# Kernel optimization log

Hardware: AMD Instinct MI355X
Metric: run time of the kernel (lower is better)

## Reference

```python
import jax, jax.numpy as jnp
import numpy as np

B, L, D, H = 2, 4096, 1024, 4
DK = D // H
DV = D // H
CHUNK, FIRS, FIRL, CONV, GROUP = 32, 3, 31, 4, 2
EPS_ID, R_EPS = 0.06, 0.025   # step==0 -> router epsilon at its start value
R_HID = 2 * D
R_IN = D + H * 6


def _l2norm(x, eps=1e-6):
    return x * jax.lax.rsqrt(jnp.sum(x * x, -1, keepdims=True) + eps)


def _causal_dwconv(x, w):
    # x: (b, l, c), w: (c, k); depthwise causal conv1d
    c = x.shape[-1]
    k = w.shape[-1]
    lhs = jnp.swapaxes(x, 1, 2)              # (b, c, l)
    rhs = w[:, None, :]                      # (c, 1, k)
    y = jax.lax.conv_general_dilated(lhs, rhs, window_strides=(1,), padding=[(k - 1, 0)],
                                     dimension_numbers=('NCH', 'OIH', 'NCH'), feature_group_count=c)
    return jnp.swapaxes(y, 1, 2)


def _fir(x, filt):
    # x: (b, l, h, d), filt: (h, d, k) depthwise causal FIR per head-channel
    b, l, h, d = x.shape
    y = _causal_dwconv(x.reshape(b, l, h * d), filt.reshape(h * d, -1))
    return y.reshape(b, l, h, d)


def _delta_rule_chunkwise(q, k, v, beta, chunk=CHUNK):
    # q,k: (b,h,L,dk)  v: (b,h,L,dv)  beta: (b,h,L); L % chunk == 0
    b, h, Ls, dk = q.shape
    dv = v.shape[-1]
    n = Ls // chunk
    q = _l2norm(q)
    k = _l2norm(k)
    v = v * beta[..., None]
    kb = k * beta[..., None]
    rs = lambda t: t.reshape(b, h, n, chunk, -1)
    q, k, v, kb = map(rs, (q, k, v, kb))
    tri = jnp.triu(jnp.ones((chunk, chunk), bool), 0)
    # UT transform: forward substitution to invert (I + strictly-lower(K_beta K^T))
    T = jnp.where(tri, 0.0, -(kb @ jnp.swapaxes(k, -1, -2)))
    for i in range(1, chunk):
        T = T.at[..., i, :].add(jnp.einsum('...j,...jl->...l', T[..., i, :], T))
    T = T + jnp.eye(chunk, dtype=T.dtype)
    u = T @ v          # (b,h,n,c,dv)
    w = T @ kb         # (b,h,n,c,dk)
    fmask = jnp.triu(jnp.ones((chunk, chunk), bool), 1)
    mv = lambda t: jnp.moveaxis(t, 2, 0)

    def step(S, xs):
        qi, ki, ui, wi = xs
        attn = jnp.where(fmask, 0.0, qi @ jnp.swapaxes(ki, -1, -2))
        u2 = ui - wi @ S
        oi = qi @ S + attn @ u2
        return S + jnp.swapaxes(ki, -1, -2) @ u2, oi

    S0 = jnp.zeros((b, h, dk, dv), q.dtype)
    S, o = jax.lax.scan(step, S0, (mv(q), mv(k), mv(u), mv(w)))
    return jnp.moveaxis(o, 0, 2).reshape(b, h, Ls, dv), S


def setup_inputs():
    key = jax.random.key(0)
    ks = jax.random.split(key, 20)
    lin = lambda kk, i, o: 0.02 * jax.random.normal(kk, (i, o), jnp.float32)

    def fir(kk, kern):
        base = jnp.zeros((H, DV, kern), jnp.float32).at[:, :, -1].set(1.0)
        return base + 0.01 * jax.random.normal(kk, (H, DV, kern), jnp.float32)

    return {
        'hidden_states': jax.random.normal(ks[0], (B, L, D), jnp.float32),
        'Wq': lin(ks[1], D, H * DK), 'Wk': lin(ks[2], D, H * DK), 'Wv': lin(ks[3], D, H * DV),
        'Wb': lin(ks[4], D, H),
        'conv_q': 0.3 * jax.random.normal(ks[5], (H * DK, CONV), jnp.float32),
        'conv_k': 0.3 * jax.random.normal(ks[6], (H * DK, CONV), jnp.float32),
        'conv_v': 0.3 * jax.random.normal(ks[7], (H * DV, CONV), jnp.float32),
        'fir_short': fir(ks[8], FIRS), 'fir_long': fir(ks[9], FIRL),
        'alpha_id': jnp.zeros((H,), jnp.float32),
        'Wid': lin(ks[10], D, H), 'bid': jnp.zeros((H,), jnp.float32),
        'Wr1': lin(ks[11], R_IN, R_HID), 'br1': jnp.zeros((R_HID,), jnp.float32),
        'Wr2': lin(ks[12], R_HID, H * 3), 'br2': jnp.zeros((H * 3,), jnp.float32),
        'log_tau_group': jnp.zeros(((H + GROUP - 1) // GROUP,), jnp.float32),
        'log_tau_head': jnp.zeros((H,), jnp.float32),
        'o_norm_w': jnp.ones((DV,), jnp.float32),
        'Wo': lin(ks[13], H * DV, D),
    }


def reference(hidden_states, Wq, Wk, Wv, Wb, conv_q, conv_k, conv_v, fir_short, fir_long,
              alpha_id, Wid, bid, Wr1, br1, Wr2, br2, log_tau_group, log_tau_head, o_norm_w, Wo):
    x = hidden_states
    b, l = x.shape[:2]
    # projections + causal short conv + silu (qk_activation='silu')
    q = jax.nn.silu(_causal_dwconv(x @ Wq, conv_q))
    k = jax.nn.silu(_causal_dwconv(x @ Wk, conv_k))
    v = jax.nn.silu(_causal_dwconv(x @ Wv, conv_v))
    qh = q.reshape(b, l, H, DK)
    kh = k.reshape(b, l, H, DK)
    vh = v.reshape(b, l, H, DV)
    beta = jax.nn.sigmoid(x @ Wb)                      # (b,l,h)
    bhld = lambda t: jnp.transpose(t, (0, 2, 1, 3))
    delta, _S = _delta_rule_chunkwise(bhld(qh), bhld(kh), bhld(vh), jnp.transpose(beta, (0, 2, 1)))
    delta = jnp.transpose(delta, (0, 2, 1, 3))         # (b,l,h,dv)
    fs = _fir(vh, fir_short)
    fl = _fir(vh, fir_long)
    # per-head mean/std stats of the three branch outputs
    stats = jnp.concatenate([fs.mean(-1), fs.std(-1), fl.mean(-1), fl.std(-1),
                             delta.mean(-1), delta.std(-1)], -1)   # (b,l,6h)
    router_in = jnp.concatenate([x, stats], -1)
    hmid = jax.nn.gelu(router_in @ Wr1 + br1, approximate=False)
    logits = (hmid @ Wr2 + br2).reshape(b, l, H, 3)
    group_idx = jnp.arange(H) // GROUP
    # step==0 -> mix=1.0: tau is the per-group temperature
    tau = jnp.exp(log_tau_group)[group_idx] + 0.0 * jnp.exp(log_tau_head)
    p = jax.nn.softmax(logits / tau[None, None, :, None], -1)
    p = p * (1.0 - 3.0 * R_EPS) + R_EPS                # epsilon-floor
    o = p[..., 0:1] * fs + p[..., 1:2] * fl + p[..., 2:3] * delta
    # gated identity (value) path
    id_scale = EPS_ID + jax.nn.sigmoid(alpha_id)[None, None, :] * jax.nn.sigmoid(x @ Wid + bid)
    o = o + id_scale[..., None] * vh
    # per-head RMSNorm then output projection
    o = o * jax.lax.rsqrt(jnp.mean(o * o, -1, keepdims=True) + 1e-5) * o_norm_w
    return o.reshape(b, l, H * DV) @ Wo
```

## Files before the change

kernel.cpp:

```cpp
#include <hip/hip_runtime.h>
#include <hip/hip_bf16.h>
#include <math.h>

#define BATCH 2
#define SEQ 4096
#define DMODEL 1024
#define NH 4
#define DHEAD 256
#define NCHUNK 128
#define ROWS (BATCH * SEQ)

typedef short s8v __attribute__((ext_vector_type(8)));
typedef float f4v __attribute__((ext_vector_type(4)));

__device__ __forceinline__ float sigm(float x) { return 1.0f / (1.0f + expf(-x)); }
__device__ __forceinline__ float siluf(float x) { return x / (1.0f + expf(-x)); }
__device__ __forceinline__ unsigned short f2b(float f) {
  __hip_bfloat16 h = __float2bfloat16(f);
  return *(unsigned short*)&h;
}

__global__ __launch_bounds__(256) void cast_bf16(
    const float* __restrict__ in, __hip_bfloat16* __restrict__ out) {
  long i = ((long)blockIdx.x * 256 + threadIdx.x) * 4;
  float4 v = *(const float4*)(in + i);
  __hip_bfloat16 tmp[4] = {__float2bfloat16(v.x), __float2bfloat16(v.y),
                           __float2bfloat16(v.z), __float2bfloat16(v.w)};
  *(ushort4*)(out + i) = *(ushort4*)tmp;
}

__global__ __launch_bounds__(256) void transpose_cast(
    const float* __restrict__ W, __hip_bfloat16* __restrict__ Wt,
    int K, int N, int Ks) {
  __shared__ float tile[32][33];
  const int t = threadIdx.x;
  const int tx = t & 31, ty = t >> 5;
  const int kb = blockIdx.y * 32, nb = blockIdx.x * 32;
#pragma unroll
  for (int r = 0; r < 4; ++r) {
    int kk = kb + ty + 8 * r;
    tile[ty + 8 * r][tx] = (kk < K) ? W[(long)kk * N + nb + tx] : 0.f;
  }
  __syncthreads();
#pragma unroll
  for (int r = 0; r < 4; ++r) {
    Wt[(long)(nb + ty + 8 * r) * Ks + kb + tx] = __float2bfloat16(tile[tx][ty + 8 * r]);
  }
}

__global__ __launch_bounds__(256) void fir_transpose(
    const float* __restrict__ fshort, const float* __restrict__ flong,
    float* __restrict__ fsT, float* __restrict__ flT) {
  const int j = blockIdx.x;
  const int t = threadIdx.x;
  if (j < 31) {
#pragma unroll
    for (int i = 0; i < 4; ++i) {
      int c = t * 4 + i;
      flT[j * 1024 + c] = flong[c * 31 + j];
    }
  } else {
    int tp = j - 31;
#pragma unroll
    for (int i = 0; i < 4; ++i) {
      int c = t * 4 + i;
      fsT[tp * 1024 + c] = fshort[c * 3 + tp];
    }
  }
}

template <int ACT, bool BF16OUT>
__global__ __launch_bounds__(256) void gemm_bf16(
    const __hip_bfloat16* __restrict__ A, const __hip_bfloat16* __restrict__ Bt,
    const float* __restrict__ bias, void* __restrict__ Cv,
    int M, int N, int Ks) {
  __shared__ short As[128 * 32];
  __shared__ short Bs[128 * 32];
  const int t = threadIdx.x;
  const int wv = t >> 6;
  const int lane = t & 63;
  const int row0 = blockIdx.y * 128, col0 = blockIdx.x * 128;
  const int mq = (wv >> 1) * 64, nq = (wv & 1) * 64;
  const int ln15 = lane & 15;
  const int kq = (lane >> 4) * 8;
  const int sr = t >> 2;
  const int sc = (t & 3) * 8;
  const short* Ag = (const short*)A + (long)(row0 + sr) * Ks + sc;
  const short* Bg = (const short*)Bt + (long)(col0 + sr) * Ks + sc;
  const long rstep = (long)64 * Ks;

  f4v acc[4][4];
#pragma unroll
  for (int i = 0; i < 4; ++i)
#pragma unroll
    for (int j = 0; j < 4; ++j) acc[i][j] = (f4v){0.f, 0.f, 0.f, 0.f};

  uint4 a0 = *(const uint4*)(Ag);
  uint4 a1 = *(const uint4*)(Ag + rstep);
  uint4 b0 = *(const uint4*)(Bg);
  uint4 b1 = *(const uint4*)(Bg + rstep);
  for (int k0 = 0; k0 < Ks; k0 += 32) {
    __syncthreads();
    *(uint4*)&As[sr * 32 + sc] = a0;
    *(uint4*)&As[(sr + 64) * 32 + sc] = a1;
    *(uint4*)&Bs[sr * 32 + sc] = b0;
    *(uint4*)&Bs[(sr + 64) * 32 + sc] = b1;
    __syncthreads();
    if (k0 + 32 < Ks) {
      a0 = *(const uint4*)(Ag + k0 + 32);
      a1 = *(const uint4*)(Ag + rstep + k0 + 32);
      b0 = *(const uint4*)(Bg + k0 + 32);
      b1 = *(const uint4*)(Bg + rstep + k0 + 32);
    }
    s8v af[4], bf[4];
#pragma unroll
    for (int mt = 0; mt < 4; ++mt)
      af[mt] = *(const s8v*)&As[(mq + mt * 16 + ln15) * 32 + kq];
#pragma unroll
    for (int nt = 0; nt < 4; ++nt)
      bf[nt] = *(const s8v*)&Bs[(nq + nt * 16 + ln15) * 32 + kq];
#pragma unroll
    for (int mt = 0; mt < 4; ++mt)
#pragma unroll
      for (int nt = 0; nt < 4; ++nt)
        acc[mt][nt] = __builtin_amdgcn_mfma_f32_16x16x32_bf16(af[mt], bf[nt], acc[mt][nt], 0, 0, 0);
  }
  const int rbase = (lane >> 4) * 4;
#pragma unroll
  for (int mt = 0; mt < 4; ++mt) {
#pragma unroll
    for (int nt = 0; nt < 4; ++nt) {
      int gcol = col0 + nq + nt * 16 + ln15;
#pragma unroll
      for (int r = 0; r < 4; ++r) {
        int grow = row0 + mq + mt * 16 + rbase + r;
        float v = acc[mt][nt][r];
        if (ACT == 1) {
          v += bias[gcol];
          v = 0.5f * v * (1.0f + erff(v * 0.70710678118654752f));
        }
        if (BF16OUT) {
          ((__hip_bfloat16*)Cv)[(long)grow * N + gcol] = __float2bfloat16(v);
        } else {
          ((float*)Cv)[(long)grow * N + gcol] = v;
        }
      }
    }
  }
}

__global__ __launch_bounds__(256) void rowdot8(
    const float* __restrict__ x, const float* __restrict__ Wb,
    const float* __restrict__ Wid, const float* __restrict__ alpha_id,
    const float* __restrict__ bidp, float* __restrict__ beta, float* __restrict__ idsc) {
  const int row = blockIdx.x;
  const int t = threadIdx.x;
  const float* xr = x + (long)row * DMODEL;
  float ab[4] = {0, 0, 0, 0}, ai[4] = {0, 0, 0, 0};
  for (int k = t; k < DMODEL; k += 256) {
    float xv = xr[k];
    float4 wb = *(const float4*)(Wb + k * 4);
    float4 wi = *(const float4*)(Wid + k * 4);
    ab[0] = fmaf(xv, wb.x, ab[0]); ab[1] = fmaf(xv, wb.y, ab[1]);
    ab[2] = fmaf(xv, wb.z, ab[2]); ab[3] = fmaf(xv, wb.w, ab[3]);
    ai[0] = fmaf(xv, wi.x, ai[0]); ai[1] = fmaf(xv, wi.y, ai[1]);
    ai[2] = fmaf(xv, wi.z, ai[2]); ai[3] = fmaf(xv, wi.w, ai[3]);
  }
#pragma unroll
  for (int m = 1; m < 64; m <<= 1) {
#pragma unroll
    for (int hh = 0; hh < 4; ++hh) {
      ab[hh] += __shfl_xor(ab[hh], m);
      ai[hh] += __shfl_xor(ai[hh], m);
    }
  }
  __shared__ float red[4][8];
  if ((t & 63) == 0) {
    int wv = t >> 6;
#pragma unroll
    for (int hh = 0; hh < 4; ++hh) {
      red[wv][hh] = ab[hh];
      red[wv][4 + hh] = ai[hh];
    }
  }
  __syncthreads();
  if (t < 8) {
    float s = red[0][t] + red[1][t] + red[2][t] + red[3][t];
    if (t < 4) {
      beta[(long)row * NH + t] = sigm(s);
    } else {
      int hh = t - 4;
      idsc[(long)row * NH + hh] = 0.06f + sigm(alpha_id[hh]) * sigm(s + bidp[hh]);
    }
  }
}

__global__ __launch_bounds__(256) void conv_silu(
    const float* __restrict__ pre, const float* __restrict__ cw, float* __restrict__ out) {
  const int row = blockIdx.x;
  const int l = row & (SEQ - 1);
  const int t = threadIdx.x;
  const int cb = t * 4;
  float wts[4][4];
#pragma unroll
  for (int cc = 0; cc < 4; ++cc) {
    float4 w4 = *(const float4*)(cw + (cb + cc) * 4);
    wts[cc][0] = w4.x; wts[cc][1] = w4.y; wts[cc][2] = w4.z; wts[cc][3] = w4.w;
  }
  float acc[4] = {0, 0, 0, 0};
#pragma unroll
  for (int tap = 0; tap < 4; ++tap) {
    int lr = l - 3 + tap;
    if (lr >= 0) {
      float4 xv = *(const float4*)(pre + (long)(row - 3 + tap) * DMODEL + cb);
      acc[0] = fmaf(wts[0][tap], xv.x, acc[0]);
      acc[1] = fmaf(wts[1][tap], xv.y, acc[1]);
      acc[2] = fmaf(wts[2][tap], xv.z, acc[2]);
      acc[3] = fmaf(wts[3][tap], xv.w, acc[3]);
    }
  }
  float4 ov = make_float4(siluf(acc[0]), siluf(acc[1]), siluf(acc[2]), siluf(acc[3]));
  *(float4*)(out + (long)row * DMODEL + cb) = ov;
}

__global__ __launch_bounds__(256) void l2norm_qk(
    float* __restrict__ q, float* __restrict__ k, __hip_bfloat16* __restrict__ qpk) {
  const int t = threadIdx.x;
  const int unit = blockIdx.x * 4 + (t >> 6);
  const int lane = t & 63;
  const int row = unit >> 2;
  const int h = unit & 3;
  const int b = row >> 12;
  const int l = row & (SEQ - 1);
  const long base = (long)row * DMODEL + h * DHEAD + lane * 4;
  float4 q4 = *(const float4*)(q + base);
  float4 k4 = *(const float4*)(k + base);
  float sq = q4.x * q4.x + q4.y * q4.y + q4.z * q4.z + q4.w * q4.w;
  float sk = k4.x * k4.x + k4.y * k4.y + k4.z * k4.z + k4.w * k4.w;
#pragma unroll
  for (int m = 1; m < 64; m <<= 1) {
    sq += __shfl_xor(sq, m);
    sk += __shfl_xor(sk, m);
  }
  float rq = rsqrtf(sq + 1e-6f);
  float rk = rsqrtf(sk + 1e-6f);
  q4.x *= rq; q4.y *= rq; q4.z *= rq; q4.w *= rq;
  k4.x *= rk; k4.y *= rk; k4.z *= rk; k4.w *= rk;
  *(float4*)(q + base) = q4;
  *(float4*)(k + base) = k4;
  ushort4 qb;
  qb.x = f2b(q4.x); qb.y = f2b(q4.y); qb.z = f2b(q4.z); qb.w = f2b(q4.w);
  *(ushort4*)(qpk + ((long)(b * NH + h) * SEQ + l) * DHEAD + lane * 4) = qb;
}

__global__ __launch_bounds__(256) void phaseA(
    const float* __restrict__ qn, const float* __restrict__ kn, const float* __restrict__ v,
    const float* __restrict__ beta, float* __restrict__ u,
    __hip_bfloat16* __restrict__ wb16, __hip_bfloat16* __restrict__ kTb16,
    __hip_bfloat16* __restrict__ attnb16) {
  __shared__ float Ks[32][256];
  __shared__ float T[32][33];
  __shared__ float bet[32];
  const int bid = blockIdx.x;
  const int c = bid & (NCHUNK - 1);
  const int h = (bid >> 7) & 3;
  const int b = bid >> 9;
  const int bh = b * NH + h;
  const int l0 = c * 32;
  const int t = threadIdx.x;
  const int wv = t >> 6;
  const int lane = t & 63;

#pragma unroll
  for (int r = 0; r < 8; ++r) {
    int idx = t + 256 * r;
    int i = idx >> 6;
    int f = (idx & 63) * 4;
    long gq = ((long)(b * SEQ + l0 + i)) * DMODEL + h * DHEAD + f;
    *(float4*)&Ks[i][f] = *(const float4*)(kn + gq);
  }
  if (t < 32) bet[t] = beta[(long)(b * SEQ + l0 + t) * NH + h];
  __syncthreads();

  {
#pragma unroll
    for (int ii = 0; ii < 8; ++ii) {
      const int i = wv * 8 + ii;
      float4 a = *(const float4*)&Ks[i][lane * 4];
      float nbi = -bet[i];
      for (int j = 0; j < 32; ++j) {
        float val = 0.f;
        if (j < i) {
          float4 bb = *(const float4*)&Ks[j][lane * 4];
          float pd = a.x * bb.x + a.y * bb.y + a.z * bb.z + a.w * bb.w;
#pragma unroll
          for (int m = 1; m < 64; m <<= 1) pd += __shfl_xor(pd, m);
          val = nbi * pd;
        }
        if (lane == 0) T[i][j] = val;
      }
    }
  }
  __syncthreads();

  if (t < 32) {
    const int l = t;
    for (int i = 1; i < 32; ++i) {
      float s = 0.f;
      for (int j = 0; j < i; ++j) s = fmaf(T[i][j], T[j][l], s);
      T[i][l] += s;
    }
    for (int i = 0; i < 32; ++i) {
      float val = T[i][l] + (i == l ? 1.f : 0.f);
      T[i][l] = val * bet[l];
    }
  }
  __syncthreads();

  {
    const int d = t;
    float acc[32];
#pragma unroll
    for (int i = 0; i < 32; ++i) acc[i] = 0.f;
    for (int j = 0; j < 32; ++j) {
      float vv = v[((long)(b * SEQ + l0 + j)) * DMODEL + h * DHEAD + d];
#pragma unroll
      for (int i = 0; i < 32; ++i) acc[i] = fmaf(T[i][j], vv, acc[i]);
    }
    long ubase = ((long)bh * SEQ + l0) * DHEAD + d;
#pragma unroll
    for (int i = 0; i < 32; ++i) u[ubase + (long)i * DHEAD] = acc[i];
#pragma unroll
    for (int i = 0; i < 32; ++i) acc[i] = 0.f;
    for (int j = 0; j < 32; ++j) {
      float kv = Ks[j][d];
#pragma unroll
      for (int i = 0; i < 32; ++i) acc[i] = fmaf(T[i][j], kv, acc[i]);
    }
#pragma unroll
    for (int i = 0; i < 32; ++i) wb16[ubase + (long)i * DHEAD] = __float2bfloat16(acc[i]);
  }

  {
    const int s = t;
    unsigned short* kb = (unsigned short*)kTb16 + ((long)bh * NCHUNK + c) * 8192 + (long)s * 32;
#pragma unroll
    for (int i4 = 0; i4 < 8; ++i4) {
      ushort4 pk;
      pk.x = f2b(Ks[i4 * 4 + 0][s]);
      pk.y = f2b(Ks[i4 * 4 + 1][s]);
      pk.z = f2b(Ks[i4 * 4 + 2][s]);
      pk.w = f2b(Ks[i4 * 4 + 3][s]);
      *(ushort4*)(kb + i4 * 4) = pk;
    }
  }

  {
    long abase = ((long)bh * NCHUNK + c) * 1024;
#pragma unroll
    for (int ii = 0; ii < 8; ++ii) {
      const int i = wv * 8 + ii;
      const float* qrow = qn + ((long)(b * SEQ + l0 + i)) * DMODEL + h * DHEAD;
      float4 a = *(const float4*)(qrow + lane * 4);
      for (int j = 0; j < 32; ++j) {
        float val = 0.f;
        if (j <= i) {
          float4 bb = *(const float4*)&Ks[j][lane * 4];
          float pd = a.x * bb.x + a.y * bb.y + a.z * bb.z + a.w * bb.w;
#pragma unroll
          for (int m = 1; m < 64; m <<= 1) pd += __shfl_xor(pd, m);
          val = pd;
        }
        if (lane == 0) attnb16[abase + i * 32 + j] = __float2bfloat16(val);
      }
    }
  }
}

__global__ __launch_bounds__(64, 1) void phaseB(
    const __hip_bfloat16* __restrict__ qpk,
    const __hip_bfloat16* __restrict__ wb,
    const __hip_bfloat16* __restrict__ kTb,
    const __hip_bfloat16* __restrict__ attnb,
    const float* __restrict__ u, float* __restrict__ delta ) {
  __shared__ __align__(16) short St[16 * 264];
  __shared__ __align__(16) short Ut[16 * 40];
  const int bid = blockIdx.x;
  const int slice = bid & 15;
  const int bh = bid >> 4;
  const int d0 = slice * 16;
  const int t = threadIdx.x;
  const int ln15 = t & 15;
  const int qw = t >> 4;

  const short* wbase = (const short*)wb + (long)bh * SEQ * 256;
  const short* qbase = (const short*)qpk + (long)bh * SEQ * 256;
  const short* kTbase = (const short*)kTb + (long)bh * NCHUNK * 8192;
  const short* atbase = (const short*)attnb + (long)bh * NCHUNK * 1024;
  const float* ubase = u + (long)bh * SEQ * 256;
  float* dbase = delta + (long)bh * SEQ * 256;

  f4v Sacc[16];
#pragma unroll
  for (int kt = 0; kt < 16; ++kt) Sacc[kt] = (f4v){0.f, 0.f, 0.f, 0.f};

  s8v wA[2][8], kA[16], atv[2];
  float uf[2][4];
  {
#pragma unroll
    for (int mt = 0; mt < 2; ++mt)
#pragma unroll
      for (int ks = 0; ks < 8; ++ks)
        wA[mt][ks] = *(const s8v*)(wbase + (long)(mt * 16 + ln15) * 256 + ks * 32 + qw * 8);
#pragma unroll
    for (int kt = 0; kt < 16; ++kt)
      kA[kt] = *(const s8v*)(kTbase + (kt * 16 + ln15) * 32 + qw * 8);
#pragma unroll
    for (int mt = 0; mt < 2; ++mt) {
      atv[mt] = *(const s8v*)(atbase + (mt * 16 + ln15) * 32 + qw * 8);
#pragma unroll
      for (int r = 0; r < 4; ++r)
        uf[mt][r] = ubase[(long)(mt * 16 + qw * 4 + r) * 256 + d0 + ln15];
    }
  }

  for (int c = 0; c < NCHUNK; ++c) {
    const int l0 = c * 32;

    s8v qA[2][8];
#pragma unroll
    for (int mt = 0; mt < 2; ++mt)
#pragma unroll
      for (int ks = 0; ks < 8; ++ks)
        qA[mt][ks] = *(const s8v*)(qbase + (long)(l0 + mt * 16 + ln15) * 256 + ks * 32 + qw * 8);

#pragma unroll
    for (int kt = 0; kt < 16; ++kt) {
      ushort4 pk;
      pk.x = f2b(Sacc[kt][0]); pk.y = f2b(Sacc[kt][1]);
      pk.z = f2b(Sacc[kt][2]); pk.w = f2b(Sacc[kt][3]);
      *(ushort4*)&St[ln15 * 264 + kt * 16 + qw * 4] = pk;
    }
    asm volatile("s_waitcnt lgkmcnt(0)" ::: "memory");
    s8v bS[8];
#pragma unroll
    for (int ks = 0; ks < 8; ++ks)
      bS[ks] = *(const s8v*)&St[ln15 * 264 + ks * 32 + qw * 8];

    f4v dwa0 = (f4v){0.f,0.f,0.f,0.f}, dwb0 = (f4v){0.f,0.f,0.f,0.f};
    f4v dwa1 = (f4v){0.f,0.f,0.f,0.f}, dwb1 = (f4v){0.f,0.f,0.f,0.f};
#pragma unroll
    for (int ks = 0; ks < 4; ++ks) {
      dwa0 = __builtin_amdgcn_mfma_f32_16x16x32_bf16(wA[0][ks], bS[ks], dwa0, 0, 0, 0);
      dwa1 = __builtin_amdgcn_mfma_f32_16x16x32_bf16(wA[1][ks], bS[ks], dwa1, 0, 0, 0);
      dwb0 = __builtin_amdgcn_mfma_f32_16x16x32_bf16(wA[0][ks + 4], bS[ks + 4], dwb0, 0, 0, 0);
      dwb1 = __builtin_amdgcn_mfma_f32_16x16x32_bf16(wA[1][ks + 4], bS[ks + 4], dwb1, 0, 0, 0);
    }
    float u2a[4], u2b[4];
#pragma unroll
    for (int r = 0; r < 4; ++r) {
      u2a[r] = uf[0][r] - (dwa0[r] + dwb0[r]);
      u2b[r] = uf[1][r] - (dwa1[r] + dwb1[r]);
    }
    {
      ushort4 pa, pb;
      pa.x = f2b(u2a[0]); pa.y = f2b(u2a[1]); pa.z = f2b(u2a[2]); pa.w = f2b(u2a[3]);
      pb.x = f2b(u2b[0]); pb.y = f2b(u2b[1]); pb.z = f2b(u2b[2]); pb.w = f2b(u2b[3]);
      *(ushort4*)&Ut[ln15 * 40 + qw * 4] = pa;
      *(ushort4*)&Ut[ln15 * 40 + 16 + qw * 4] = pb;
    }
    asm volatile("s_waitcnt lgkmcnt(0)" ::: "memory");
    s8v bu = *(const s8v*)&Ut[ln15 * 40 + qw * 8];

    f4v oA0 = __builtin_amdgcn_mfma_f32_16x16x32_bf16(atv[0], bu, (f4v){0.f,0.f,0.f,0.f}, 0, 0, 0);
    f4v oA1 = __builtin_amdgcn_mfma_f32_16x16x32_bf16(atv[1], bu, (f4v){0.f,0.f,0.f,0.f}, 0, 0, 0);

#pragma unroll
    for (int kt = 0; kt < 16; ++kt)
      Sacc[kt] = __builtin_amdgcn_mfma_f32_16x16x32_bf16(kA[kt], bu, Sacc[kt], 0, 0, 0);

    if (c + 1 < NCHUNK) {
      const int ln = l0 + 32;
#pragma unroll
      for (int mt = 0; mt < 2; ++mt)
#pragma unroll
        for (int ks = 0; ks < 8; ++ks)
          wA[mt][ks] = *(const s8v*)(wbase + (long)(ln + mt * 16 + ln15) * 256 + ks * 32 + qw * 8);
#pragma unroll
      for (int kt = 0; kt < 16; ++kt)
        kA[kt] = *(const s8v*)(kTbase + (long)(c + 1) * 8192 + (kt * 16 + ln15) * 32 + qw * 8);
#pragma unroll
      for (int mt = 0; mt < 2; ++mt) {
        atv[mt] = *(const s8v*)(atbase + (long)(c + 1) * 1024 + (mt * 16 + ln15) * 32 + qw * 8);
#pragma unroll
        for (int r = 0; r < 4; ++r)
          uf[mt][r] = ubase[(long)(ln + mt * 16 + qw * 4 + r) * 256 + d0 + ln15];
      }
    }

    f4v oB0 = (f4v){0.f,0.f,0.f,0.f}, oB1 = (f4v){0.f,0.f,0.f,0.f};
#pragma unroll
    for (int ks = 0; ks < 4; ++ks) {
      oA0 = __builtin_amdgcn_mfma_f32_16x16x32_bf16(qA[0][ks], bS[ks], oA0, 0, 0, 0);
      oA1 = __builtin_amdgcn_mfma_f32_16x16x32_bf16(qA[1][ks], bS[ks], oA1, 0, 0, 0);
      oB0 = __builtin_amdgcn_mfma_f32_16x16x32_bf16(qA[0][ks + 4], bS[ks + 4], oB0, 0, 0, 0);
      oB1 = __builtin_amdgcn_mfma_f32_16x16x32_bf16(qA[1][ks + 4], bS[ks + 4], oB1, 0, 0, 0);
    }
#pragma unroll
    for (int r = 0; r < 4; ++r) {
      dbase[(long)(l0 + qw * 4 + r) * 256 + d0 + ln15] = oA0[r] + oB0[r];
      dbase[(long)(l0 + 16 + qw * 4 + r) * 256 + d0 + ln15] = oA1[r] + oB1[r];
    }
  }
}

__global__ __launch_bounds__(256) void fir_kernel(
    const float* __restrict__ v, const float* __restrict__ fsT,
    const float* __restrict__ flT, float* __restrict__ fs, float* __restrict__ fl) {
  const int row = blockIdx.x;
  const int l = row & (SEQ - 1);
  const int t = threadIdx.x;
  const int cb = t * 4;
  float4 accl = make_float4(0, 0, 0, 0);
  float4 accs = make_float4(0, 0, 0, 0);
  const float* vb = v + (long)(row - 30) * DMODEL + cb;
  if (l >= 30) {
#pragma unroll
    for (int j = 0; j < 31; ++j) {
      float4 w4 = *(const float4*)(flT + j * DMODEL + cb);
      float4 xv = *(const float4*)(vb + (long)j * DMODEL);
      accl.x = fmaf(w4.x, xv.x, accl.x);
      accl.y = fmaf(w4.y, xv.y, accl.y);
      accl.z = fmaf(w4.z, xv.z, accl.z);
      accl.w = fmaf(w4.w, xv.w, accl.w);
      if (j >= 28) {
        float4 s4 = *(const float4*)(fsT + (j - 28) * DMODEL + cb);
        accs.x = fmaf(s4.x, xv.x, accs.x);
        accs.y = fmaf(s4.y, xv.y, accs.y);
        accs.z = fmaf(s4.z, xv.z, accs.z);
        accs.w = fmaf(s4.w, xv.w, accs.w);
      }
    }
  } else {
    for (int j = 30 - l; j < 31; ++j) {
      float4 w4 = *(const float4*)(flT + j * DMODEL + cb);
      float4 xv = *(const float4*)(vb + (long)j * DMODEL);
      accl.x = fmaf(w4.x, xv.x, accl.x);
      accl.y = fmaf(w4.y, xv.y, accl.y);
      accl.z = fmaf(w4.z, xv.z, accl.z);
      accl.w = fmaf(w4.w, xv.w, accl.w);
      if (j >= 28) {
        float4 s4 = *(const float4*)(fsT + (j - 28) * DMODEL + cb);
        accs.x = fmaf(s4.x, xv.x, accs.x);
        accs.y = fmaf(s4.y, xv.y, accs.y);
        accs.z = fmaf(s4.z, xv.z, accs.z);
        accs.w = fmaf(s4.w, xv.w, accs.w);
      }
    }
  }
  *(float4*)(fs + (long)row * DMODEL + cb) = accs;
  *(float4*)(fl + (long)row * DMODEL + cb) = accl;
}

__global__ __launch_bounds__(256) void stats_router(
    const float* __restrict__ x, const float* __restrict__ fs,
    const float* __restrict__ fl, const float* __restrict__ dl,
    __hip_bfloat16* __restrict__ rinb) {
  const int row = blockIdx.x;
  const int b = row >> 12;
  const int l = row & (SEQ - 1);
  const int t = threadIdx.x;
  float4 xv = *(const float4*)(x + (long)row * DMODEL + t * 4);
  {
    __hip_bfloat16 tmp[4] = {__float2bfloat16(xv.x), __float2bfloat16(xv.y),
                             __float2bfloat16(xv.z), __float2bfloat16(xv.w)};
    *(ushort4*)(rinb + (long)row * 1056 + t * 4) = *(ushort4*)tmp;
  }
  if (t < 8) rinb[(long)row * 1056 + 1048 + t] = __float2bfloat16(0.f);
  const int h = t >> 6;
  const int lane = t & 63;
  const long base = (long)row * DMODEL + h * DHEAD + lane * 4;
  const long dbase = ((long)(b * NH + h) * SEQ + l) * DHEAD + lane * 4;
  float4 a = *(const float4*)(fs + base);
  float4 bq = *(const float4*)(fl + base);
  float4 cq = *(const float4*)(dl + dbase);
  float s[6];
  s[0] = a.x + a.y + a.z + a.w;
  s[1] = a.x * a.x + a.y * a.y + a.z * a.z + a.w * a.w;
  s[2] = bq.x + bq.y + bq.z + bq.w;
  s[3] = bq.x * bq.x + bq.y * bq.y + bq.z * bq.z + bq.w * bq.w;
  s[4] = cq.x + cq.y + cq.z + cq.w;
  s[5] = cq.x * cq.x + cq.y * cq.y + cq.z * cq.z + cq.w * cq.w;
#pragma unroll
  for (int m = 1; m < 64; m <<= 1)
#pragma unroll
    for (int j = 0; j < 6; ++j) s[j] += __shfl_xor(s[j], m);
  if (lane == 0) {
    __hip_bfloat16* rb = rinb + (long)row * 1056 + 1024;
    float m0 = s[0] * (1.f / 256.f);
    float m1 = s[2] * (1.f / 256.f);
    float m2 = s[4] * (1.f / 256.f);
    rb[h] = __float2bfloat16(m0);
    rb[4 + h] = __float2bfloat16(sqrtf(fmaxf(s[1] * (1.f / 256.f) - m0 * m0, 0.f)));
    rb[8 + h] = __float2bfloat16(m1);
    rb[12 + h] = __float2bfloat16(sqrtf(fmaxf(s[3] * (1.f / 256.f) - m1 * m1, 0.f)));
    rb[16 + h] = __float2bfloat16(m2);
    rb[20 + h] = __float2bfloat16(sqrtf(fmaxf(s[5] * (1.f / 256.f) - m2 * m2, 0.f)));
  }
}

__global__ __launch_bounds__(256) void router_logits(
    const __hip_bfloat16* __restrict__ hmid, const float* __restrict__ Wr2,
    const float* __restrict__ br2, const float* __restrict__ ltg, float* __restrict__ p) {
  const int row = blockIdx.x;
  const int t = threadIdx.x;
  float acc[12];
#pragma unroll
  for (int j = 0; j < 12; ++j) acc[j] = 0.f;
  const __hip_bfloat16* hr = hmid + (long)row * 2048;
  for (int k = t; k < 2048; k += 256) {
    float hv = __bfloat162float(hr[k]);
    const float* wr = Wr2 + k * 12;
#pragma unroll
    for (int j = 0; j < 12; ++j) acc[j] = fmaf(hv, wr[j], acc[j]);
  }
#pragma unroll
  for (int m = 1; m < 64; m <<= 1)
#pragma unroll
    for (int j = 0; j < 12; ++j) acc[j] += __shfl_xor(acc[j], m);
  __shared__ float red[4][12];
  if ((t & 63) == 0) {
    int wv = t >> 6;
#pragma unroll
    for (int j = 0; j < 12; ++j) red[wv][j] = acc[j];
  }
  __syncthreads();
  if (t < 4) {
    const int h = t;
    float l3[3];
#pragma unroll
    for (int j = 0; j < 3; ++j) {
      int col = h * 3 + j;
      l3[j] = red[0][col] + red[1][col] + red[2][col] + red[3][col] + br2[col];
    }
    float inv_tau = expf(-ltg[h >> 1]);
    float y0 = l3[0] * inv_tau, y1 = l3[1] * inv_tau, y2 = l3[2] * inv_tau;
    float mx = fmaxf(y0, fmaxf(y1, y2));
    float e0 = expf(y0 - mx), e1 = expf(y1 - mx), e2 = expf(y2 - mx);
    float inv = 1.f / (e0 + e1 + e2);
    p[(long)row * 12 + h * 3 + 0] = e0 * inv * 0.925f + 0.025f;
    p[(long)row * 12 + h * 3 + 1] = e1 * inv * 0.925f + 0.025f;
    p[(long)row * 12 + h * 3 + 2] = e2 * inv * 0.925f + 0.025f;
  }
}

__global__ __launch_bounds__(256) void omix(
    const float* __restrict__ fs, const float* __restrict__ fl,
    const float* __restrict__ dl, const float* __restrict__ vh,
    const float* __restrict__ p, const float* __restrict__ idsc,
    const float* __restrict__ onw, __hip_bfloat16* __restrict__ o) {
  const int row = blockIdx.x;
  const int b = row >> 12;
  const int l = row & (SEQ - 1);
  const int t = threadIdx.x;
  const int h = t >> 6;
  const int lane = t & 63;
  const long base = (long)row * DMODEL + h * DHEAD + lane * 4;
  const long dbase = ((long)(b * NH + h) * SEQ + l) * DHEAD + lane * 4;
  float p0 = p[(long)row * 12 + h * 3 + 0];
  float p1 = p[(long)row * 12 + h * 3 + 1];
  float p2 = p[(long)row * 12 + h * 3 + 2];
  float idv = idsc[(long)row * NH + h];
  float4 a = *(const float4*)(fs + base);
  float4 bq = *(const float4*)(fl + base);
  float4 cq = *(const float4*)(dl + dbase);
  float4 vv = *(const float4*)(vh + base);
  float4 ov;
  ov.x = p0 * a.x + p1 * bq.x + p2 * cq.x + idv * vv.x;
  ov.y = p0 * a.y + p1 * bq.y + p2 * cq.y + idv * vv.y;
  ov.z = p0 * a.z + p1 * bq.z + p2 * cq.z + idv * vv.z;
  ov.w = p0 * a.w + p1 * bq.w + p2 * cq.w + idv * vv.w;
  float ss = ov.x * ov.x + ov.y * ov.y + ov.z * ov.z + ov.w * ov.w;
#pragma unroll
  for (int m = 1; m < 64; m <<= 1) ss += __shfl_xor(ss, m);
  float rms = rsqrtf(ss * (1.f / 256.f) + 1e-5f);
  float4 wn = *(const float4*)(onw + lane * 4);
  __hip_bfloat16 tmp[4] = {__float2bfloat16(ov.x * rms * wn.x),
                           __float2bfloat16(ov.y * rms * wn.y),
                           __float2bfloat16(ov.z * rms * wn.z),
                           __float2bfloat16(ov.w * rms * wn.w)};
  *(ushort4*)(o + base) = *(ushort4*)tmp;
}

extern "C" void kernel_launch(void* const* d_in, const int* in_sizes, int n_in,
                              void* d_out, int out_size, void* d_ws, size_t ws_size,
                              hipStream_t stream) {
  const float* x = (const float*)d_in[0];
  const float* Wq = (const float*)d_in[1];
  const float* Wk = (const float*)d_in[2];
  const float* Wv = (const float*)d_in[3];
  const float* Wb = (const float*)d_in[4];
  const float* conv_q = (const float*)d_in[5];
  const float* conv_k = (const float*)d_in[6];
  const float* conv_v = (const float*)d_in[7];
  const float* fir_s = (const float*)d_in[8];
  const float* fir_l = (const float*)d_in[9];
  const float* alpha_id = (const float*)d_in[10];
  const float* Wid = (const float*)d_in[11];
  const float* bidp = (const float*)d_in[12];
  const float* Wr1 = (const float*)d_in[13];
  const float* br1 = (const float*)d_in[14];
  const float* Wr2 = (const float*)d_in[15];
  const float* br2 = (const float*)d_in[16];
  const float* ltg = (const float*)d_in[17];
  const float* onw = (const float*)d_in[19];
  const float* Wo = (const float*)d_in[20];

  float* ws = (float*)d_ws;
  float* pre = ws + 0;
  float* ubuf = ws + 8388608;
  float* wbuf = ws + 16777216;
  float* attnbuf = ws + 25165824;
  float* qbuf = ws + 26214400;
  float* kbuf = ws + 34603008;
  float* vbuf = ws + 42991616;
  float* betabuf = ws + 51380224;
  float* idscbuf = ws + 51412992;
  float* pbuf = ws + 51445760;
  float* flTb = ws + 51544064;
  float* fsTb = ws + 51575808;
  float* deltabuf = ubuf;
  __hip_bfloat16* xb = (__hip_bfloat16*)ubuf;
  __hip_bfloat16* Wqt = (__hip_bfloat16*)(wbuf);
  __hip_bfloat16* Wkt = (__hip_bfloat16*)(wbuf + 524288);
  __hip_bfloat16* Wvt = (__hip_bfloat16*)(wbuf + 1048576);
  __hip_bfloat16* wb16 = (__hip_bfloat16*)wbuf;
  __hip_bfloat16* kTb16 = (__hip_bfloat16*)wbuf + 8388608;
  __hip_bfloat16* attnb16 = (__hip_bfloat16*)attnbuf;
  __hip_bfloat16* qpk16 = (__hip_bfloat16*)pre;
  __hip_bfloat16* rinb = (__hip_bfloat16*)(wbuf);
  __hip_bfloat16* Wr1t = (__hip_bfloat16*)(wbuf + 4325376);
  __hip_bfloat16* Wot = (__hip_bfloat16*)(wbuf + 5406720);
  __hip_bfloat16* omixb = (__hip_bfloat16*)(wbuf);
  __hip_bfloat16* hmid = (__hip_bfloat16*)pre;
  float* fsb = qbuf;
  float* flb = kbuf;

  dim3 blk(256);
  cast_bf16<<<dim3(ROWS), blk, 0, stream>>>(x, xb);
  transpose_cast<<<dim3(32, 32), blk, 0, stream>>>(Wq, Wqt, 1024, 1024, 1024);
  transpose_cast<<<dim3(32, 32), blk, 0, stream>>>(Wk, Wkt, 1024, 1024, 1024);
  transpose_cast<<<dim3(32, 32), blk, 0, stream>>>(Wv, Wvt, 1024, 1024, 1024);
  fir_transpose<<<dim3(34), blk, 0, stream>>>(fir_s, fir_l, fsTb, flTb);
  gemm_bf16<0, false><<<dim3(8, 64), blk, 0, stream>>>(xb, Wqt, nullptr, pre, ROWS, 1024, 1024);
  conv_silu<<<dim3(ROWS), blk, 0, stream>>>(pre, conv_q, qbuf);
  gemm_bf16<0, false><<<dim3(8, 64), blk, 0, stream>>>(xb, Wkt, nullptr, pre, ROWS, 1024, 1024);
  conv_silu<<<dim3(ROWS), blk, 0, stream>>>(pre, conv_k, kbuf);
  gemm_bf16<0, false><<<dim3(8, 64), blk, 0, stream>>>(xb, Wvt, nullptr, pre, ROWS, 1024, 1024);
  conv_silu<<<dim3(ROWS), blk, 0, stream>>>(pre, conv_v, vbuf);
  rowdot8<<<dim3(ROWS), blk, 0, stream>>>(x, Wb, Wid, alpha_id, bidp, betabuf, idscbuf);
  l2norm_qk<<<dim3(ROWS), blk, 0, stream>>>(qbuf, kbuf, qpk16);
  phaseA<<<dim3(BATCH * NH * NCHUNK), blk, 0, stream>>>(qbuf, kbuf, vbuf, betabuf, ubuf, wb16, kTb16, attnb16);
  phaseB<<<dim3(BATCH * NH * 16), dim3(64), 0, stream>>>(qpk16, wb16, kTb16, attnb16, ubuf, deltabuf);
  fir_kernel<<<dim3(ROWS), blk, 0, stream>>>(vbuf, fsTb, flTb, fsb, flb);
  stats_router<<<dim3(ROWS), blk, 0, stream>>>(x, fsb, flb, deltabuf, rinb);
  transpose_cast<<<dim3(64, 33), blk, 0, stream>>>(Wr1, Wr1t, 1048, 2048, 1056);
  transpose_cast<<<dim3(32, 32), blk, 0, stream>>>(Wo, Wot, 1024, 1024, 1024);
  gemm_bf16<1, true><<<dim3(16, 64), blk, 0, stream>>>(rinb, Wr1t, br1, hmid, ROWS, 2048, 1056);
  router_logits<<<dim3(ROWS), blk, 0, stream>>>(hmid, Wr2, br2, ltg, pbuf);
  omix<<<dim3(ROWS), blk, 0, stream>>>(fsb, flb, deltabuf, vbuf, pbuf, idscbuf, onw, omixb);
  gemm_bf16<0, false><<<dim3(8, 64), blk, 0, stream>>>(omixb, Wot, nullptr, d_out, ROWS, 1024, 1024);
}
```

Before: 970.6 us.

## Fuse l2norm into conv, merge beta/id into cast, use split-bf16 MFMA in phaseA

Merges the x-to-bf16 cast with the beta and identity-gate row dot products into one kernel. It also folds the per-head L2 normalization of q and k into the conv+SiLU epilogue, with each 64-lane wave covering one head, which removes the separate l2norm pass. In phaseA the K K^T and Q K^T products now run on bf16 MFMA with hi/lo splitting for near-fp32 accuracy, replacing per-element wave shuffle reductions. Shared memory now stores k as bf16 hi/lo pairs, and the q bf16 pack is written inside phaseA.

New measurement: 851.6 us. 1.14x faster.

```diff
diff --git a/kernel.cpp b/kernel.cpp
--- a/kernel.cpp
+++ b/kernel.cpp
@@ -19,14 +19,64 @@
   __hip_bfloat16 h = __float2bfloat16(f);
   return *(unsigned short*)&h;
 }
-
-__global__ __launch_bounds__(256) void cast_bf16(
-    const float* __restrict__ in, __hip_bfloat16* __restrict__ out) {
-  long i = ((long)blockIdx.x * 256 + threadIdx.x) * 4;
-  float4 v = *(const float4*)(in + i);
-  __hip_bfloat16 tmp[4] = {__float2bfloat16(v.x), __float2bfloat16(v.y),
-                           __float2bfloat16(v.z), __float2bfloat16(v.w)};
-  *(ushort4*)(out + i) = *(ushort4*)tmp;
+__device__ __forceinline__ float b2f(unsigned short u) {
+  __hip_bfloat16 h = *(__hip_bfloat16*)&u;
+  return __bfloat162float(h);
+}
+
+__global__ __launch_bounds__(256) void prep_x(
+    const float* __restrict__ x, __hip_bfloat16* __restrict__ xb,
+    const float* __restrict__ Wb, const float* __restrict__ Wid,
+    const float* __restrict__ alpha_id, const float* __restrict__ bidp,
+    float* __restrict__ beta, float* __restrict__ idsc) {
+  const int row = blockIdx.x;
+  const int t = threadIdx.x;
+  const long base = (long)row * DMODEL + t * 4;
+  float4 xv = *(const float4*)(x + base);
+  {
+    __hip_bfloat16 tmp[4] = {__float2bfloat16(xv.x), __float2bfloat16(xv.y),
+                             __float2bfloat16(xv.z), __float2bfloat16(xv.w)};
+    *(ushort4*)(xb + base) = *(ushort4*)tmp;
+  }
+  float xa[4] = {xv.x, xv.y, xv.z, xv.w};
+  float ab[4] = {0, 0, 0, 0}, ai[4] = {0, 0, 0, 0};
+#pragma unroll
+  for (int i = 0; i < 4; ++i) {
+    int k = t * 4 + i;
+    float4 wb4 = *(const float4*)(Wb + k * 4);
+    float4 wi4 = *(const float4*)(Wid + k * 4);
+    ab[0] = fmaf(xa[i], wb4.x, ab[0]); ab[1] = fmaf(xa[i], wb4.y, ab[1]);
+    ab[2] = fmaf(xa[i], wb4.z, ab[2]); ab[3] = fmaf(xa[i], wb4.w, ab[3]);
+    ai[0] = fmaf(xa[i], wi4.x, ai[0]); ai[1] = fmaf(xa[i], wi4.y, ai[1]);
+    ai[2] = fmaf(xa[i], wi4.z, ai[2]); ai[3] = fmaf(xa[i], wi4.w, ai[3]);
+  }
+#pragma unroll
+  for (int m = 1; m < 64; m <<= 1) {
+#pragma unroll
+    for (int hh = 0; hh < 4; ++hh) {
+      ab[hh] += __shfl_xor(ab[hh], m);
+      ai[hh] += __shfl_xor(ai[hh], m);
+    }
+  }
+  __shared__ float red[4][8];
+  if ((t & 63) == 0) {
+    int wv = t >> 6;
+#pragma unroll
+    for (int hh = 0; hh < 4; ++hh) {
+      red[wv][hh] = ab[hh];
+      red[wv][4 + hh] = ai[hh];
+    }
+  }
+  __syncthreads();
+  if (t < 8) {
+    float s = red[0][t] + red[1][t] + red[2][t] + red[3][t];
+    if (t < 4) {
+      beta[(long)row * NH + t] = sigm(s);
+    } else {
+      int hh = t - 4;
+      idsc[(long)row * NH + hh] = 0.06f + sigm(alpha_id[hh]) * sigm(s + bidp[hh]);
+    }
+  }
 }
 
 __global__ __launch_bounds__(256) void transpose_cast(
@@ -149,52 +199,7 @@
   }
 }
 
-__global__ __launch_bounds__(256) void rowdot8(
-    const float* __restrict__ x, const float* __restrict__ Wb,
-    const float* __restrict__ Wid, const float* __restrict__ alpha_id,
-    const float* __restrict__ bidp, float* __restrict__ beta, float* __restrict__ idsc) {
-  const int row = blockIdx.x;
-  const int t = threadIdx.x;
-  const float* xr = x + (long)row * DMODEL;
-  float ab[4] = {0, 0, 0, 0}, ai[4] = {0, 0, 0, 0};
-  for (int k = t; k < DMODEL; k += 256) {
-    float xv = xr[k];
-    float4 wb = *(const float4*)(Wb + k * 4);
-    float4 wi = *(const float4*)(Wid + k * 4);
-    ab[0] = fmaf(xv, wb.x, ab[0]); ab[1] = fmaf(xv, wb.y, ab[1]);
-    ab[2] = fmaf(xv, wb.z, ab[2]); ab[3] = fmaf(xv, wb.w, ab[3]);
-    ai[0] = fmaf(xv, wi.x, ai[0]); ai[1] = fmaf(xv, wi.y, ai[1]);
-    ai[2] = fmaf(xv, wi.z, ai[2]); ai[3] = fmaf(xv, wi.w, ai[3]);
-  }
-#pragma unroll
-  for (int m = 1; m < 64; m <<= 1) {
-#pragma unroll
-    for (int hh = 0; hh < 4; ++hh) {
-      ab[hh] += __shfl_xor(ab[hh], m);
-      ai[hh] += __shfl_xor(ai[hh], m);
-    }
-  }
-  __shared__ float red[4][8];
-  if ((t & 63) == 0) {
-    int wv = t >> 6;
-#pragma unroll
-    for (int hh = 0; hh < 4; ++hh) {
-      red[wv][hh] = ab[hh];
-      red[wv][4 + hh] = ai[hh];
-    }
-  }
-  __syncthreads();
-  if (t < 8) {
-    float s = red[0][t] + red[1][t] + red[2][t] + red[3][t];
-    if (t < 4) {
-      beta[(long)row * NH + t] = sigm(s);
-    } else {
-      int hh = t - 4;
-      idsc[(long)row * NH + hh] = 0.06f + sigm(alpha_id[hh]) * sigm(s + bidp[hh]);
-    }
-  }
-}
-
+template <int MODE>
 __global__ __launch_bounds__(256) void conv_silu(
     const float* __restrict__ pre, const float* __restrict__ cw, float* __restrict__ out) {
   const int row = blockIdx.x;
@@ -219,46 +224,27 @@
       acc[3] = fmaf(wts[3][tap], xv.w, acc[3]);
     }
   }
-  float4 ov = make_float4(siluf(acc[0]), siluf(acc[1]), siluf(acc[2]), siluf(acc[3]));
+#pragma unroll
+  for (int i = 0; i < 4; ++i) acc[i] = siluf(acc[i]);
+  if (MODE == 1) {
+    float ss = acc[0] * acc[0] + acc[1] * acc[1] + acc[2] * acc[2] + acc[3] * acc[3];
+#pragma unroll
+    for (int m = 1; m < 64; m <<= 1) ss += __shfl_xor(ss, m);
+    float rn = rsqrtf(ss + 1e-6f);
+#pragma unroll
+    for (int i = 0; i < 4; ++i) acc[i] *= rn;
+  }
+  float4 ov = make_float4(acc[0], acc[1], acc[2], acc[3]);
   *(float4*)(out + (long)row * DMODEL + cb) = ov;
-}
-
-__global__ __launch_bounds__(256) void l2norm_qk(
-    float* __restrict__ q, float* __restrict__ k, __hip_bfloat16* __restrict__ qpk) {
-  const int t = threadIdx.x;
-  const int unit = blockIdx.x * 4 + (t >> 6);
-  const int lane = t & 63;
-  const int row = unit >> 2;
-  const int h = unit & 3;
-  const int b = row >> 12;
-  const int l = row & (SEQ - 1);
-  const long base = (long)row * DMODEL + h * DHEAD + lane * 4;
-  float4 q4 = *(const float4*)(q + base);
-  float4 k4 = *(const float4*)(k + base);
-  float sq = q4.x * q4.x + q4.y * q4.y + q4.z * q4.z + q4.w * q4.w;
-  float sk = k4.x * k4.x + k4.y * k4.y + k4.z * k4.z + k4.w * k4.w;
-#pragma unroll
-  for (int m = 1; m < 64; m <<= 1) {
-    sq += __shfl_xor(sq, m);
-    sk += __shfl_xor(sk, m);
-  }
-  float rq = rsqrtf(sq + 1e-6f);
-  float rk = rsqrtf(sk + 1e-6f);
-  q4.x *= rq; q4.y *= rq; q4.z *= rq; q4.w *= rq;
-  k4.x *= rk; k4.y *= rk; k4.z *= rk; k4.w *= rk;
-  *(float4*)(q + base) = q4;
-  *(float4*)(k + base) = k4;
-  ushort4 qb;
-  qb.x = f2b(q4.x); qb.y = f2b(q4.y); qb.z = f2b(q4.z); qb.w = f2b(q4.w);
-  *(ushort4*)(qpk + ((long)(b * NH + h) * SEQ + l) * DHEAD + lane * 4) = qb;
 }
 
 __global__ __launch_bounds__(256) void phaseA(
     const float* __restrict__ qn, const float* __restrict__ kn, const float* __restrict__ v,
     const float* __restrict__ beta, float* __restrict__ u,
     __hip_bfloat16* __restrict__ wb16, __hip_bfloat16* __restrict__ kTb16,
-    __hip_bfloat16* __restrict__ attnb16) {
-  __shared__ float Ks[32][256];
+    __hip_bfloat16* __restrict__ attnb16, __hip_bfloat16* __restrict__ qpk) {
+  __shared__ short khi[32 * 264];
+  __shared__ short klo[32 * 264];
   __shared__ float T[32][33];
   __shared__ float bet[32];
   const int bid = blockIdx.x;
@@ -270,35 +256,94 @@
   const int t = threadIdx.x;
   const int wv = t >> 6;
   const int lane = t & 63;
+  const int ln15 = lane & 15;
+  const int qw = lane >> 4;
 
 #pragma unroll
   for (int r = 0; r < 8; ++r) {
     int idx = t + 256 * r;
     int i = idx >> 6;
     int f = (idx & 63) * 4;
-    long gq = ((long)(b * SEQ + l0 + i)) * DMODEL + h * DHEAD + f;
-    *(float4*)&Ks[i][f] = *(const float4*)(kn + gq);
+    float4 kv = *(const float4*)(kn + ((long)(b * SEQ + l0 + i)) * DMODEL + h * DHEAD + f);
+    float a[4] = {kv.x, kv.y, kv.z, kv.w};
+    ushort4 hi4, lo4;
+    unsigned short* hp = (unsigned short*)&hi4;
+    unsigned short* lp = (unsigned short*)&lo4;
+#pragma unroll
+    for (int j = 0; j < 4; ++j) {
+      unsigned short hb = f2b(a[j]);
+      hp[j] = hb;
+      lp[j] = f2b(a[j] - b2f(hb));
+    }
+    *(ushort4*)&khi[i * 264 + f] = hi4;
+    *(ushort4*)&klo[i * 264 + f] = lo4;
   }
   if (t < 32) bet[t] = beta[(long)(b * SEQ + l0 + t) * NH + h];
   __syncthreads();
 
-  {
-#pragma unroll
-    for (int ii = 0; ii < 8; ++ii) {
-      const int i = wv * 8 + ii;
-      float4 a = *(const float4*)&Ks[i][lane * 4];
-      float nbi = -bet[i];
-      for (int j = 0; j < 32; ++j) {
-        float val = 0.f;
-        if (j < i) {
-          float4 bb = *(const float4*)&Ks[j][lane * 4];
-          float pd = a.x * bb.x + a.y * bb.y + a.z * bb.z + a.w * bb.w;
-#pragma unroll
-          for (int m = 1; m < 64; m <<= 1) pd += __shfl_xor(pd, m);
-          val = nbi * pd;
-        }
-        if (lane == 0) T[i][j] = val;
+  if (wv < 2) {
+    const int mt = wv;
+    f4v acc0 = (f4v){0.f, 0.f, 0.f, 0.f};
+    f4v acc1 = (f4v){0.f, 0.f, 0.f, 0.f};
+#pragma unroll
+    for (int ks = 0; ks < 8; ++ks) {
+      s8v ahi = *(const s8v*)&khi[(mt * 16 + ln15) * 264 + ks * 32 + qw * 8];
+      s8v alo = *(const s8v*)&klo[(mt * 16 + ln15) * 264 + ks * 32 + qw * 8];
+      s8v bhi0 = *(const s8v*)&khi[ln15 * 264 + ks * 32 + qw * 8];
+      s8v blo0 = *(const s8v*)&klo[ln15 * 264 + ks * 32 + qw * 8];
+      s8v bhi1 = *(const s8v*)&khi[(16 + ln15) * 264 + ks * 32 + qw * 8];
+      s8v blo1 = *(const s8v*)&klo[(16 + ln15) * 264 + ks * 32 + qw * 8];
+      acc0 = __builtin_amdgcn_mfma_f32_16x16x32_bf16(ahi, bhi0, acc0, 0, 0, 0);
+      acc0 = __builtin_amdgcn_mfma_f32_16x16x32_bf16(ahi, blo0, acc0, 0, 0, 0);
+      acc0 = __builtin_amdgcn_mfma_f32_16x16x32_bf16(alo, bhi0, acc0, 0, 0, 0);
+      acc1 = __builtin_amdgcn_mfma_f32_16x16x32_bf16(ahi, bhi1, acc1, 0, 0, 0);
+      acc1 = __builtin_amdgcn_mfma_f32_16x16x32_bf16(ahi, blo1, acc1, 0, 0, 0);
+      acc1 = __builtin_amdgcn_mfma_f32_16x16x32_bf16(alo, bhi1, acc1, 0, 0, 0);
+    }
+#pragma unroll
+    for (int r = 0; r < 4; ++r) {
+      int i = mt * 16 + qw * 4 + r;
+      int j0 = ln15, j1 = 16 + ln15;
+      T[i][j0] = (j0 < i) ? -bet[i] * acc0[r] : 0.f;
+      T[i][j1] = (j1 < i) ? -bet[i] * acc1[r] : 0.f;
+    }
+  } else {
+    const int mt = wv - 2;
+    const long qoff = (long)(b * SEQ + l0 + mt * 16 + ln15) * DMODEL + h * DHEAD;
+    __hip_bfloat16* qdst = qpk + ((long)bh * SEQ + l0 + mt * 16 + ln15) * DHEAD;
+    f4v acc0 = (f4v){0.f, 0.f, 0.f, 0.f};
+    f4v acc1 = (f4v){0.f, 0.f, 0.f, 0.f};
+#pragma unroll
+    for (int ks = 0; ks < 8; ++ks) {
+      float4 q0 = *(const float4*)(qn + qoff + ks * 32 + qw * 8);
+      float4 q1 = *(const float4*)(qn + qoff + ks * 32 + qw * 8 + 4);
+      float a8[8] = {q0.x, q0.y, q0.z, q0.w, q1.x, q1.y, q1.z, q1.w};
+      s8v ahi, alo;
+#pragma unroll
+      for (int j = 0; j < 8; ++j) {
+        unsigned short hb = f2b(a8[j]);
+        ahi[j] = (short)hb;
+        alo[j] = (short)f2b(a8[j] - b2f(hb));
       }
+      *(s8v*)(qdst + ks * 32 + qw * 8) = ahi;
+      s8v bhi0 = *(const s8v*)&khi[ln15 * 264 + ks * 32 + qw * 8];
+      s8v blo0 = *(const s8v*)&klo[ln15 * 264 + ks * 32 + qw * 8];
+      s8v bhi1 = *(const s8v*)&khi[(16 + ln15) * 264 + ks * 32 + qw * 8];
+      s8v blo1 = *(const s8v*)&klo[(16 + ln15) * 264 + ks * 32 + qw * 8];
+      acc0 = __builtin_amdgcn_mfma_f32_16x16x32_bf16(ahi, bhi0, acc0, 0, 0, 0);
+      acc0 = __builtin_amdgcn_mfma_f32_16x16x32_bf16(ahi, blo0, acc0, 0, 0, 0);
+      acc0 = __builtin_amdgcn_mfma_f32_16x16x32_bf16(alo, bhi0, acc0, 0, 0, 0);
+      acc1 = __builtin_amdgcn_mfma_f32_16x16x32_bf16(ahi, bhi1, acc1, 0, 0, 0);
+      acc1 = __builtin_amdgcn_mfma_f32_16x16x32_bf16(ahi, blo1, acc1, 0, 0, 0);
+      acc1 = __builtin_amdgcn_mfma_f32_16x16x32_bf16(alo, bhi1, acc1, 0, 0, 0);
+    }
+    long abase = ((long)bh * NCHUNK + c) * 1024;
+#pragma unroll
+    for (int r = 0; r < 4; ++r) {
+      int i = mt * 16 + qw * 4 + r;
+      int j0 = ln15, j1 = 16 + ln15;
+      attnb16[abase + i * 32 + j0] = __float2bfloat16(j0 <= i ? acc0[r] : 0.f);
+      attnb16[abase + i * 32 + j1] = __float2bfloat16(j1 <= i ? acc1[r] : 0.f);
     }
   }
   __syncthreads();
@@ -333,7 +378,7 @@
 #pragma unroll
     for (int i = 0; i < 32; ++i) acc[i] = 0.f;
     for (int j = 0; j < 32; ++j) {
-      float kv = Ks[j][d];
+      float kv = b2f((unsigned short)khi[j * 264 + d]) + b2f((unsigned short)klo[j * 264 + d]);
 #pragma unroll
       for (int i = 0; i < 32; ++i) acc[i] = fmaf(T[i][j], kv, acc[i]);
     }
@@ -347,32 +392,11 @@
 #pragma unroll
     for (int i4 = 0; i4 < 8; ++i4) {
       ushort4 pk;
-      pk.x = f2b(Ks[i4 * 4 + 0][s]);
-      pk.y = f2b(Ks[i4 * 4 + 1][s]);
-      pk.z = f2b(Ks[i4 * 4 + 2][s]);
-      pk.w = f2b(Ks[i4 * 4 + 3][s]);
+      pk.x = (unsigned short)khi[(i4 * 4 + 0) * 264 + s];
+      pk.y = (unsigned short)khi[(i4 * 4 + 1) * 264 + s];
+      pk.z = (unsigned short)khi[(i4 * 4 + 2) * 264 + s];
+      pk.w = (unsigned short)khi[(i4 * 4 + 3) * 264 + s];
       *(ushort4*)(kb + i4 * 4) = pk;
-    }
-  }
-
-  {
-    long abase = ((long)bh * NCHUNK + c) * 1024;
-#pragma unroll
-    for (int ii = 0; ii < 8; ++ii) {
-      const int i = wv * 8 + ii;
-      const float* qrow = qn + ((long)(b * SEQ + l0 + i)) * DMODEL + h * DHEAD;
-      float4 a = *(const float4*)(qrow + lane * 4);
-      for (int j = 0; j < 32; ++j) {
-        float val = 0.f;
-        if (j <= i) {
-          float4 bb = *(const float4*)&Ks[j][lane * 4];
-          float pd = a.x * bb.x + a.y * bb.y + a.z * bb.z + a.w * bb.w;
-#pragma unroll
-          for (int m = 1; m < 64; m <<= 1) pd += __shfl_xor(pd, m);
-          val = pd;
-        }
-        if (lane == 0) attnb16[abase + i * 32 + j] = __float2bfloat16(val);
-      }
     }
   }
 }
@@ -747,20 +771,18 @@
   float* flb = kbuf;
 
   dim3 blk(256);
-  cast_bf16<<<dim3(ROWS), blk, 0, stream>>>(x, xb);
+  prep_x<<<dim3(ROWS), blk, 0, stream>>>(x, xb, Wb, Wid, alpha_id, bidp, betabuf, idscbuf);
   transpose_cast<<<dim3(32, 32), blk, 0, stream>>>(Wq, Wqt, 1024, 1024, 1024);
   transpose_cast<<<dim3(32, 32), blk, 0, stream>>>(Wk, Wkt, 1024, 1024, 1024);
   transpose_cast<<<dim3(32, 32), blk, 0, stream>>>(Wv, Wvt, 1024, 1024, 1024);
   fir_transpose<<<dim3(34), blk, 0, stream>>>(fir_s, fir_l, fsTb, flTb);
   gemm_bf16<0, false><<<dim3(8, 64), blk, 0, stream>>>(xb, Wqt, nullptr, pre, ROWS, 1024, 1024);
-  conv_silu<<<dim3(ROWS), blk, 0, stream>>>(pre, conv_q, qbuf);
+  conv_silu<1><<<dim3(ROWS), blk, 0, stream>>>(pre, conv_q, qbuf);
   gemm_bf16<0, false><<<dim3(8, 64), blk, 0, stream>>>(xb, Wkt, nullptr, pre, ROWS, 1024, 1024);
-  conv_silu<<<dim3(ROWS), blk, 0, stream>>>(pre, conv_k, kbuf);
+  conv_silu<1><<<dim3(ROWS), blk, 0, stream>>>(pre, conv_k, kbuf);
   gemm_bf16<0, false><<<dim3(8, 64), blk, 0, stream>>>(xb, Wvt, nullptr, pre, ROWS, 1024, 1024);
-  conv_silu<<<dim3(ROWS), blk, 0, stream>>>(pre, conv_v, vbuf);
-  rowdot8<<<dim3(ROWS), blk, 0, stream>>>(x, Wb, Wid, alpha_id, bidp, betabuf, idscbuf);
-  l2norm_qk<<<dim3(ROWS), blk, 0, stream>>>(qbuf, kbuf, qpk16);
-  phaseA<<<dim3(BATCH * NH * NCHUNK), blk, 0, stream>>>(qbuf, kbuf, vbuf, betabuf, ubuf, wb16, kTb16, attnb16);
+  conv_silu<0><<<dim3(ROWS), blk, 0, stream>>>(pre, conv_v, vbuf);
+  phaseA<<<dim3(BATCH * NH * NCHUNK), blk, 0, stream>>>(qbuf, kbuf, vbuf, betabuf, ubuf, wb16, kTb16, attnb16, qpk16);
   phaseB<<<dim3(BATCH * NH * 16), dim3(64), 0, stream>>>(qpk16, wb16, kTb16, attnb16, ubuf, deltabuf);
   fir_kernel<<<dim3(ROWS), blk, 0, stream>>>(vbuf, fsTb, flTb, fsb, flb);
   stats_router<<<dim3(ROWS), blk, 0, stream>>>(x, fsb, flb, deltabuf, rinb);
```
